# Performance work log

Measured on AMD Instinct MI355X. Metric: run time of the kernel, lower is better.

Reference implementation:

```python
import jax, jax.numpy as jnp
import numpy as np

B, N, D_IN, H, MSG, L, TGT, N_LAYERS = 8, 1024, 64, 128, 128, 5, 12, 3


def setup_inputs() -> dict:
    key = jax.random.key(0)
    ks = jax.random.split(key, 10)
    g = jax.random.uniform(ks[0], (B, N, N), jnp.float32)          # adjacency / edge weights
    h_in = jax.random.uniform(ks[1], (B, N, D_IN), jnp.float32)    # node features (positive -> all nodes present)
    e = jax.random.randint(ks[2], (B, N, N), 0, L).astype(jnp.int32)  # discrete edge labels in [0, L)

    def init(k, shape, fan):
        return jax.random.normal(k, shape, jnp.float32) / np.sqrt(fan)

    A = init(ks[3], (L, H, MSG), H)            # per-edge-label message matrices
    Wi = init(ks[4], (MSG, 3 * H), MSG)        # GRU input weights (r,z,n)
    Wh = init(ks[5], (H, 3 * H), H)            # GRU hidden weights (r,z,n)
    bi = jnp.zeros((3 * H,), jnp.float32)
    bh = jnp.zeros((3 * H,), jnp.float32)
    W_gate = init(ks[6], (2 * H, TGT), 2 * H)  # readout gating net i([h_T, h_0])
    b_gate = jnp.zeros((TGT,), jnp.float32)
    W_out = init(ks[7], (H, TGT), H)           # readout net j(h_T)
    b_out = jnp.zeros((TGT,), jnp.float32)
    return dict(g=g, h_in=h_in, e=e, A=A, Wi=Wi, Wh=Wh, bi=bi, bh=bh,
                W_gate=W_gate, b_gate=b_gate, W_out=W_out, b_out=b_out)


def _gru_step(m, h, Wi, Wh, bi, bh):
    # Single GRU step applied independently per node: m [B,N,MSG], h [B,N,H]
    gi = m @ Wi + bi
    gh = h @ Wh + bh
    i_r, i_z, i_n = jnp.split(gi, 3, axis=-1)
    h_r, h_z, h_n = jnp.split(gh, 3, axis=-1)
    r = jax.nn.sigmoid(i_r + h_r)
    z = jax.nn.sigmoid(i_z + h_z)
    n = jnp.tanh(i_n + r * h_n)
    return (1.0 - z) * n + z * h


def reference(g, h_in, e, A, Wi, Wh, bi, bh, W_gate, b_gate, W_out, b_out):
    n_labels, hidden = A.shape[0], A.shape[1]
    # pad input features with zeros up to hidden_state_size
    h0 = jnp.pad(h_in, ((0, 0), (0, 0), (0, hidden - h_in.shape[-1])))
    # node-presence mask: sum(|h_in|) > 0  -> [B,N,1]
    node_mask = (jnp.sum(jnp.abs(h_in), axis=-1, keepdims=True) > 0).astype(h0.dtype)
    h = h0
    for _ in range(N_LAYERS):  # weight-tied message passing
        # per-label candidate messages: M_l[b,w,:] = h[b,w,:] @ A_l  -> [L,B,N,MSG]
        Ml = jnp.einsum('bwd,ldo->lbwo', h, A)
        agg = jnp.zeros(h.shape[:2] + (A.shape[2],), h.dtype)
        for l in range(n_labels):
            # mask by adjacency AND matching edge label, sum over neighbors w
            w_l = g * (e == l).astype(g.dtype)                  # [B,N,N]
            agg = agg + jnp.einsum('bvw,bwo->bvo', w_l, Ml[l])  # [B,N,MSG]
        h = _gru_step(agg, h, Wi, Wh, bi, bh) * node_mask
    hT = h
    # GGNN readout: sum_v sigmoid(i([h_T, h_0])) * j(h_T), masked on present nodes
    gate = jax.nn.sigmoid(jnp.concatenate([hT, h0], axis=-1) @ W_gate + b_gate)
    out = gate * (hT @ W_out + b_out)                            # [B,N,TGT]
    read_mask = (jnp.sum(h0, axis=-1, keepdims=True) > 0).astype(h0.dtype)
    return jnp.sum(out * read_mask, axis=1)                      # [B,TGT]
```

## Files before the change

### kernel.cpp

```cpp
#include <hip/hip_runtime.h>

#define B_      8
#define N_      1024
#define DIN_    64
#define H_      128
#define MSG2    128
#define L_      5
#define TGT_    12
#define NLAYERS_ 3
#define CAT_    640
#define NODES   (B_ * N_)
#define KSPLIT  4

typedef __attribute__((ext_vector_type(8))) short s16x8;
typedef __attribute__((ext_vector_type(4))) float f32x4;

__device__ __forceinline__ float sigmoidf_(float x) { return 1.f / (1.f + __expf(-x)); }

__device__ __forceinline__ unsigned short f2bf(float x) {
  unsigned int u = __float_as_uint(x);
  u += 0x7FFFu + ((u >> 16) & 1u);
  return (unsigned short)(u >> 16);
}
__device__ __forceinline__ float bf2f(unsigned short u) {
  return __uint_as_float(((unsigned int)u) << 16);
}

__global__ __launch_bounds__(256) void k_prep(const float* __restrict__ h_in,
                                              const float* __restrict__ A,
                                              const float* __restrict__ Wi,
                                              const float* __restrict__ Wh,
                                              float* __restrict__ h,
                                              float* __restrict__ h0,
                                              unsigned short* __restrict__ X,
                                              float* __restrict__ maskA,
                                              float* __restrict__ maskR,
                                              unsigned short* __restrict__ ATh,
                                              unsigned short* __restrict__ ATl,
                                              unsigned short* __restrict__ WiTh,
                                              unsigned short* __restrict__ WiTl,
                                              unsigned short* __restrict__ WhTh,
                                              unsigned short* __restrict__ WhTl) {
  const int blk = blockIdx.x;
  if (blk < NODES / 4) {
    int node = blk * 4 + (threadIdx.x >> 6);
    int lane = threadIdx.x & 63;
    float v = h_in[(size_t)node * DIN_ + lane];
    size_t base = (size_t)node * H_;
    h[base + lane] = v;   h[base + 64 + lane] = 0.f;
    h0[base + lane] = v;  h0[base + 64 + lane] = 0.f;
    unsigned short hi = f2bf(v);
    unsigned short lo = f2bf(v - bf2f(hi));
    size_t xb = (size_t)node * 256;
    X[xb + lane] = hi;        X[xb + 64 + lane] = 0;
    X[xb + 128 + lane] = lo;  X[xb + 192 + lane] = 0;
    float sa = fabsf(v), ss = v;
    for (int off = 32; off > 0; off >>= 1) {
      sa += __shfl_down(sa, off);
      ss += __shfl_down(ss, off);
    }
    if (lane == 0) {
      maskA[node] = (sa > 0.f) ? 1.f : 0.f;
      maskR[node] = (ss > 0.f) ? 1.f : 0.f;
    }
  } else if (blk < NODES / 4 + (CAT_ * 128) / 256) {
    int idx = (blk - NODES / 4) * 256 + threadIdx.x;
    int c = idx >> 7, d = idx & 127;
    int l = c >> 7, o = c & 127;
    float v = A[((size_t)l * 128 + d) * 128 + o];
    unsigned short hi = f2bf(v);
    ATh[idx] = hi;
    ATl[idx] = f2bf(v - bf2f(hi));
  } else {
    int idx = (blk - NODES / 4 - (CAT_ * 128) / 256) * 256 + threadIdx.x;
    if (idx < 384 * 128) {
      int c = idx >> 7, k = idx & 127;
      float v = Wi[(size_t)k * 384 + c];
      unsigned short hi = f2bf(v);
      WiTh[idx] = hi; WiTl[idx] = f2bf(v - bf2f(hi));
    } else {
      int i = idx - 384 * 128;
      int c = i >> 7, k = i & 127;
      float v = Wh[(size_t)k * 384 + c];
      unsigned short hi = f2bf(v);
      WhTh[i] = hi; WhTl[i] = f2bf(v - bf2f(hi));
    }
  }
}

__global__ __launch_bounds__(256) void k_pack(const float* __restrict__ g,
                                              const int* __restrict__ e,
                                              unsigned short* __restrict__ Gb,
                                              unsigned char* __restrict__ Eb) {
  size_t i8 = ((size_t)blockIdx.x * 256 + threadIdx.x) * 8;
  float4 g0 = *(const float4*)&g[i8];
  float4 g1 = *(const float4*)&g[i8 + 4];
  int4   e0 = *(const int4*)&e[i8];
  int4   e1 = *(const int4*)&e[i8 + 4];
  ushort4 ga, gb;
  ga.x = f2bf(g0.x); ga.y = f2bf(g0.y); ga.z = f2bf(g0.z); ga.w = f2bf(g0.w);
  gb.x = f2bf(g1.x); gb.y = f2bf(g1.y); gb.z = f2bf(g1.z); gb.w = f2bf(g1.w);
  *(ushort4*)&Gb[i8]     = ga;
  *(ushort4*)&Gb[i8 + 4] = gb;
  uint2 ev;
  ev.x = (unsigned)(e0.x & 0xFF) | ((unsigned)(e0.y & 0xFF) << 8) |
         ((unsigned)(e0.z & 0xFF) << 16) | ((unsigned)(e0.w & 0xFF) << 24);
  ev.y = (unsigned)(e1.x & 0xFF) | ((unsigned)(e1.y & 0xFF) << 8) |
         ((unsigned)(e1.z & 0xFF) << 16) | ((unsigned)(e1.w & 0xFF) << 24);
  *(uint2*)&Eb[i8] = ev;
}

__global__ __launch_bounds__(256) void k_gemmT(const unsigned short* __restrict__ X,
                                               const unsigned short* __restrict__ ATh,
                                               const unsigned short* __restrict__ ATl,
                                               unsigned short* __restrict__ McatT) {
  __shared__ __align__(16) unsigned short Ah[64 * 40];
  __shared__ __align__(16) unsigned short Al[64 * 40];
  __shared__ __align__(16) unsigned short Bh[128 * 40];
  __shared__ __align__(16) unsigned short Bl2[128 * 40];
  const int tid = threadIdx.x;
  const int c0 = blockIdx.x * 128;
  const int node0 = blockIdx.y * 64;
  const int b = node0 >> 10;
  const int w0 = node0 & 1023;
  const int wid = tid >> 6, lane = tid & 63;
  const int wr = wid >> 1, wc = wid & 1;
  const int lr = lane & 15, lg = lane >> 4;
  const int ar = tid >> 2, aq = (tid & 3) * 8;
  const int br = tid >> 1, bq = (tid & 1) * 16;
  f32x4 acc[2][4];
  #pragma unroll
  for (int m = 0; m < 2; ++m)
    #pragma unroll
    for (int n = 0; n < 4; ++n) acc[m][n] = {0.f, 0.f, 0.f, 0.f};
  for (int kk = 0; kk < 4; ++kk) {
    const int kb = kk * 32;
    *(uint4*)&Ah[ar * 40 + aq] = *(const uint4*)&X[(size_t)(node0 + ar) * 256 + kb + aq];
    *(uint4*)&Al[ar * 40 + aq] = *(const uint4*)&X[(size_t)(node0 + ar) * 256 + 128 + kb + aq];
    const unsigned short* bh = ATh + (size_t)(c0 + br) * 128 + kb + bq;
    const unsigned short* bl = ATl + (size_t)(c0 + br) * 128 + kb + bq;
    *(uint4*)&Bh[br * 40 + bq]      = *(const uint4*)bh;
    *(uint4*)&Bh[br * 40 + bq + 8]  = *(const uint4*)(bh + 8);
    *(uint4*)&Bl2[br * 40 + bq]     = *(const uint4*)bl;
    *(uint4*)&Bl2[br * 40 + bq + 8] = *(const uint4*)(bl + 8);
    __syncthreads();
    s16x8 ah[2], al[2], bhf[4], blf[4];
    #pragma unroll
    for (int m = 0; m < 2; ++m) {
      int row = (wr * 32 + m * 16 + lr) * 40 + lg * 8;
      ah[m] = *(const s16x8*)&Ah[row];
      al[m] = *(const s16x8*)&Al[row];
    }
    #pragma unroll
    for (int n = 0; n < 4; ++n) {
      int row = (wc * 64 + n * 16 + lr) * 40 + lg * 8;
      bhf[n] = *(const s16x8*)&Bh[row];
      blf[n] = *(const s16x8*)&Bl2[row];
    }
    #pragma unroll
    for (int m = 0; m < 2; ++m)
      #pragma unroll
      for (int n = 0; n < 4; ++n) {
        acc[m][n] = __builtin_amdgcn_mfma_f32_16x16x32_bf16(ah[m], bhf[n], acc[m][n], 0, 0, 0);
        acc[m][n] = __builtin_amdgcn_mfma_f32_16x16x32_bf16(ah[m], blf[n], acc[m][n], 0, 0, 0);
        acc[m][n] = __builtin_amdgcn_mfma_f32_16x16x32_bf16(al[m], bhf[n], acc[m][n], 0, 0, 0);
      }
    __syncthreads();
  }
  #pragma unroll
  for (int m = 0; m < 2; ++m)
    #pragma unroll
    for (int n = 0; n < 4; ++n) {
      int c = c0 + wc * 64 + n * 16 + lr;
      int l = c >> 7, o = c & 127;
      int w = w0 + wr * 32 + m * 16 + lg * 4;
      ushort4 v;
      v.x = f2bf(acc[m][n][0]); v.y = f2bf(acc[m][n][1]);
      v.z = f2bf(acc[m][n][2]); v.w = f2bf(acc[m][n][3]);
      *(ushort4*)&McatT[(((size_t)b * L_ + l) * MSG2 + o) * N_ + w] = v;
    }
}

__global__ __launch_bounds__(256, 4) void k_agg_mfma(const unsigned short* __restrict__ Gb,
                                                     const unsigned char* __restrict__ Eb,
                                                     const unsigned short* __restrict__ McatT,
                                                     float* __restrict__ aggP) {
  __shared__ __align__(16) unsigned short Gm[L_][64 * 32];
  __shared__ __align__(16) unsigned short Bl[L_][64 * 32];
  char* GmB = (char*)Gm;
  char* BlB = (char*)Bl;

  const int tid = threadIdx.x;
  const int fid = blockIdx.x;
  const int xcd = fid & 7;
  const int s   = fid >> 3;
  const int p   = xcd * 4 + (s >> 5);
  const int idx = s & 31;
  const int v0  = (idx & 15) * 64;
  const int oh  = idx >> 4;
  const int ks  = p >> 3;
  const int b   = p & 7;

  const int wid  = tid >> 6, lane = tid & 63;
  const int wr   = wid >> 1, wc = wid & 1;
  const int lr   = lane & 15, lg = lane >> 4;

  f32x4 acc[2][2];
  #pragma unroll
  for (int m = 0; m < 2; ++m)
    #pragma unroll
    for (int n = 0; n < 2; ++n) acc[m][n] = {0.f, 0.f, 0.f, 0.f};

  const int ar = tid >> 2, aq = (tid & 3) * 8;
  const int br = tid >> 2, bq = (tid & 3) * 8;
  const size_t garow = ((size_t)b * N_ + v0 + ar) * N_;
  const size_t mrowb = (((size_t)b * L_) * MSG2 + oh * 64 + br) * N_;
  const size_t lstep = (size_t)MSG2 * N_;
  const int ksbase = ks * 256;

  const int gt_w = (ar * 64 + aq * 2) ^ ((ar & 7) << 4);
  const int bl_w = (br * 64 + bq * 2) ^ ((br & 7) << 4);
  const int fsw  = (lr & 7) << 4;

  for (int kk = 0; kk < 8; ++kk) {
    const int kb = ksbase + kk * 32;
    s16x8 gs = *(const s16x8*)&Gb[garow + kb + aq];
    uint2 ev = *(const uint2*)&Eb[garow + kb + aq];
    uint4 bv[L_];
    #pragma unroll
    for (int l = 0; l < L_; ++l)
      bv[l] = *(const uint4*)(McatT + mrowb + (size_t)l * lstep + kb + bq);
    {
      unsigned int w0e = ev.x, w1e = ev.y;
      #pragma unroll
      for (int l = 0; l < L_; ++l) {
        s16x8 mg;
        mg[0] = (((w0e      ) & 0xFFu) == (unsigned)l) ? gs[0] : (short)0;
        mg[1] = (((w0e >>  8) & 0xFFu) == (unsigned)l) ? gs[1] : (short)0;
        mg[2] = (((w0e >> 16) & 0xFFu) == (unsigned)l) ? gs[2] : (short)0;
        mg[3] = (((w0e >> 24) & 0xFFu) == (unsigned)l) ? gs[3] : (short)0;
        mg[4] = (((w1e      ) & 0xFFu) == (unsigned)l) ? gs[4] : (short)0;
        mg[5] = (((w1e >>  8) & 0xFFu) == (unsigned)l) ? gs[5] : (short)0;
        mg[6] = (((w1e >> 16) & 0xFFu) == (unsigned)l) ? gs[6] : (short)0;
        mg[7] = (((w1e >> 24) & 0xFFu) == (unsigned)l) ? gs[7] : (short)0;
        *(s16x8*)(GmB + l * 4096 + gt_w) = mg;
      }
    }
    #pragma unroll
    for (int l = 0; l < L_; ++l)
      *(uint4*)(BlB + l * (64 * 64) + bl_w) = bv[l];
    __syncthreads();

    #pragma unroll
    for (int l = 0; l < L_; ++l) {
      s16x8 af[2], bfr[2];
      #pragma unroll
      for (int m = 0; m < 2; ++m) {
        int row = wr * 32 + m * 16 + lr;
        af[m] = *(const s16x8*)(GmB + l * 4096 + ((row * 64 + lg * 16) ^ fsw));
      }
      #pragma unroll
      for (int n = 0; n < 2; ++n) {
        int row = wc * 32 + n * 16 + lr;
        bfr[n] = *(const s16x8*)(BlB + l * (64 * 64) + ((row * 64 + lg * 16) ^ fsw));
      }
      #pragma unroll
      for (int m = 0; m < 2; ++m)
        #pragma unroll
        for (int n = 0; n < 2; ++n)
          acc[m][n] = __builtin_amdgcn_mfma_f32_16x16x32_bf16(af[m], bfr[n], acc[m][n], 0, 0, 0);
    }
    __syncthreads();
  }

  float* op = aggP + ((size_t)ks * NODES + (size_t)b * N_ + v0) * MSG2 + oh * 64;
  #pragma unroll
  for (int m = 0; m < 2; ++m)
    #pragma unroll
    for (int n = 0; n < 2; ++n)
      #pragma unroll
      for (int j = 0; j < 4; ++j) {
        int row = wr * 32 + m * 16 + lg * 4 + j;
        int col = wc * 32 + n * 16 + lr;
        op[(size_t)row * MSG2 + col] = acc[m][n][j];
      }
}

__global__ __launch_bounds__(256) void k_gates_mfma(const float* __restrict__ aggP,
                                                    const unsigned short* __restrict__ Xh,
                                                    const unsigned short* __restrict__ WiTh,
                                                    const unsigned short* __restrict__ WiTl,
                                                    const unsigned short* __restrict__ WhTh,
                                                    const unsigned short* __restrict__ WhTl,
                                                    float* __restrict__ gates) {
  __shared__ __align__(16) unsigned short Ah[64 * 40];
  __shared__ __align__(16) unsigned short Al[64 * 40];
  __shared__ __align__(16) unsigned short Bh[128 * 40];
  __shared__ __align__(16) unsigned short Bl2[128 * 40];
  const int tid = threadIdx.x;
  const int z = blockIdx.z;
  const unsigned short* WTh = z ? WhTh : WiTh;
  const unsigned short* WTl = z ? WhTl : WiTl;
  const int c0 = blockIdx.x * 128;
  const int node0 = blockIdx.y * 64;
  const int wid = tid >> 6, lane = tid & 63;
  const int wr = wid >> 1, wc = wid & 1;
  const int lr = lane & 15, lg = lane >> 4;
  const int ar = tid >> 2, aq = (tid & 3) * 8;
  const int br = tid >> 1, bq = (tid & 1) * 16;
  const size_t slab = (size_t)NODES * MSG2;
  f32x4 acc[2][4];
  #pragma unroll
  for (int m = 0; m < 2; ++m)
    #pragma unroll
    for (int n = 0; n < 4; ++n) acc[m][n] = {0.f, 0.f, 0.f, 0.f};
  for (int kk = 0; kk < 4; ++kk) {
    const int kb = kk * 32;
    if (z == 0) {
      const float* ap = aggP + (size_t)(node0 + ar) * MSG2 + kb + aq;
      float sv[8] = {0.f, 0.f, 0.f, 0.f, 0.f, 0.f, 0.f, 0.f};
      #pragma unroll
      for (int ss = 0; ss < KSPLIT; ++ss) {
        float4 x0 = *(const float4*)(ap + (size_t)ss * slab);
        float4 x1 = *(const float4*)(ap + (size_t)ss * slab + 4);
        sv[0] += x0.x; sv[1] += x0.y; sv[2] += x0.z; sv[3] += x0.w;
        sv[4] += x1.x; sv[5] += x1.y; sv[6] += x1.z; sv[7] += x1.w;
      }
      s16x8 hv, lv;
      #pragma unroll
      for (int j = 0; j < 8; ++j) {
        unsigned short hi = f2bf(sv[j]);
        hv[j] = (short)hi;
        lv[j] = (short)f2bf(sv[j] - bf2f(hi));
      }
      *(s16x8*)&Ah[ar * 40 + aq] = hv;
      *(s16x8*)&Al[ar * 40 + aq] = lv;
    } else {
      *(uint4*)&Ah[ar * 40 + aq] = *(const uint4*)&Xh[(size_t)(node0 + ar) * 256 + kb + aq];
      *(uint4*)&Al[ar * 40 + aq] = *(const uint4*)&Xh[(size_t)(node0 + ar) * 256 + 128 + kb + aq];
    }
    const unsigned short* bh = WTh + (size_t)(c0 + br) * 128 + kb + bq;
    const unsigned short* bl = WTl + (size_t)(c0 + br) * 128 + kb + bq;
    *(uint4*)&Bh[br * 40 + bq]      = *(const uint4*)bh;
    *(uint4*)&Bh[br * 40 + bq + 8]  = *(const uint4*)(bh + 8);
    *(uint4*)&Bl2[br * 40 + bq]     = *(const uint4*)bl;
    *(uint4*)&Bl2[br * 40 + bq + 8] = *(const uint4*)(bl + 8);
    __syncthreads();
    s16x8 ah[2], al[2], bhf[4], blf[4];
    #pragma unroll
    for (int m = 0; m < 2; ++m) {
      int row = (wr * 32 + m * 16 + lr) * 40 + lg * 8;
      ah[m] = *(const s16x8*)&Ah[row];
      al[m] = *(const s16x8*)&Al[row];
    }
    #pragma unroll
    for (int n = 0; n < 4; ++n) {
      int row = (wc * 64 + n * 16 + lr) * 40 + lg * 8;
      bhf[n] = *(const s16x8*)&Bh[row];
      blf[n] = *(const s16x8*)&Bl2[row];
    }
    #pragma unroll
    for (int m = 0; m < 2; ++m)
      #pragma unroll
      for (int n = 0; n < 4; ++n) {
        acc[m][n] = __builtin_amdgcn_mfma_f32_16x16x32_bf16(ah[m], bhf[n], acc[m][n], 0, 0, 0);
        acc[m][n] = __builtin_amdgcn_mfma_f32_16x16x32_bf16(ah[m], blf[n], acc[m][n], 0, 0, 0);
        acc[m][n] = __builtin_amdgcn_mfma_f32_16x16x32_bf16(al[m], bhf[n], acc[m][n], 0, 0, 0);
      }
    __syncthreads();
  }
  #pragma unroll
  for (int m = 0; m < 2; ++m)
    #pragma unroll
    for (int n = 0; n < 4; ++n) {
      int c = c0 + wc * 64 + n * 16 + lr;
      int row = node0 + wr * 32 + m * 16 + lg * 4;
      #pragma unroll
      for (int j = 0; j < 4; ++j)
        gates[(size_t)(row + j) * 768 + z * 384 + c] = acc[m][n][j];
    }
}

__global__ __launch_bounds__(256) void k_gru_elt(const float* __restrict__ gates,
                                                 const float* __restrict__ bi,
                                                 const float* __restrict__ bh,
                                                 const float* __restrict__ maskA,
                                                 float* __restrict__ h,
                                                 unsigned short* __restrict__ X,
                                                 int writeX) {
  const int t = threadIdx.x;
  const int node = blockIdx.x * 8 + (t >> 5);
  const int j4 = (t & 31) * 4;
  const size_t gb = (size_t)node * 768;
  float4 gir = *(const float4*)&gates[gb + j4];
  float4 giz = *(const float4*)&gates[gb + 128 + j4];
  float4 gin = *(const float4*)&gates[gb + 256 + j4];
  float4 ghr = *(const float4*)&gates[gb + 384 + j4];
  float4 ghz = *(const float4*)&gates[gb + 512 + j4];
  float4 ghn = *(const float4*)&gates[gb + 640 + j4];
  float4 bir = *(const float4*)&bi[j4];
  float4 biz = *(const float4*)&bi[128 + j4];
  float4 bin = *(const float4*)&bi[256 + j4];
  float4 bhr = *(const float4*)&bh[j4];
  float4 bhz = *(const float4*)&bh[128 + j4];
  float4 bhn = *(const float4*)&bh[256 + j4];
  float4 hv = *(const float4*)&h[(size_t)node * 128 + j4];
  float m = maskA[node];
  float4 ho;
  {
    float r = sigmoidf_(gir.x + bir.x + ghr.x + bhr.x);
    float z = sigmoidf_(giz.x + biz.x + ghz.x + bhz.x);
    float nn = tanhf(gin.x + bin.x + r * (ghn.x + bhn.x));
    ho.x = ((1.f - z) * nn + z * hv.x) * m;
  }
  {
    float r = sigmoidf_(gir.y + bir.y + ghr.y + bhr.y);
    float z = sigmoidf_(giz.y + biz.y + ghz.y + bhz.y);
    float nn = tanhf(gin.y + bin.y + r * (ghn.y + bhn.y));
    ho.y = ((1.f - z) * nn + z * hv.y) * m;
  }
  {
    float r = sigmoidf_(gir.z + bir.z + ghr.z + bhr.z);
    float z = sigmoidf_(giz.z + biz.z + ghz.z + bhz.z);
    float nn = tanhf(gin.z + bin.z + r * (ghn.z + bhn.z));
    ho.z = ((1.f - z) * nn + z * hv.z) * m;
  }
  {
    float r = sigmoidf_(gir.w + bir.w + ghr.w + bhr.w);
    float z = sigmoidf_(giz.w + biz.w + ghz.w + bhz.w);
    float nn = tanhf(gin.w + bin.w + r * (ghn.w + bhn.w));
    ho.w = ((1.f - z) * nn + z * hv.w) * m;
  }
  *(float4*)&h[(size_t)node * 128 + j4] = ho;
  if (writeX) {
    ushort4 hi, lo;
    hi.x = f2bf(ho.x); lo.x = f2bf(ho.x - bf2f(hi.x));
    hi.y = f2bf(ho.y); lo.y = f2bf(ho.y - bf2f(hi.y));
    hi.z = f2bf(ho.z); lo.z = f2bf(ho.z - bf2f(hi.z));
    hi.w = f2bf(ho.w); lo.w = f2bf(ho.w - bf2f(hi.w));
    *(ushort4*)&X[(size_t)node * 256 + j4]       = hi;
    *(ushort4*)&X[(size_t)node * 256 + 128 + j4] = lo;
  }
}

__global__ __launch_bounds__(256) void k_readP(const float* __restrict__ h,
                                               const float* __restrict__ h0,
                                               const float* __restrict__ Wg,
                                               const float* __restrict__ Wo,
                                               float* __restrict__ PT) {
  __shared__ float Xt[64][65];
  __shared__ float Wt[64][25];
  const int tid = threadIdx.x;
  const int node0 = blockIdx.x * 64;
  const int row = tid >> 2;
  const int cg  = tid & 3;
  float acc[6] = {0.f, 0.f, 0.f, 0.f, 0.f, 0.f};
  const int sr = tid >> 2;
  const int sk = (tid & 3) * 16;
  #pragma unroll
  for (int kb = 0; kb < 4; ++kb) {
    const float* src = (kb < 2 ? h : h0) + (size_t)(node0 + sr) * 128 + (kb & 1) * 64 + sk;
    #pragma unroll
    for (int q = 0; q < 4; ++q)
      *(float4*)&Xt[sr][sk + q * 4] = *(const float4*)(src + q * 4);
    #pragma unroll
    for (int j = 0; j < 6; ++j) {
      int idx = tid * 6 + j;
      int rk = idx / 24;
      int c24 = idx - rk * 24;
      int gk = kb * 64 + rk;
      float wv;
      if (c24 < 12) wv = Wg[(size_t)gk * TGT_ + c24];
      else          wv = (gk < 128) ? Wo[(size_t)gk * TGT_ + (c24 - 12)] : 0.f;
      Wt[rk][c24] = wv;
    }
    __syncthreads();
    #pragma unroll 8
    for (int k = 0; k < 64; ++k) {
      float x = Xt[row][k];
      #pragma unroll
      for (int j = 0; j < 6; ++j)
        acc[j] += x * Wt[k][cg * 6 + j];
    }
    __syncthreads();
  }
  #pragma unroll
  for (int j = 0; j < 6; ++j)
    PT[(size_t)(cg * 6 + j) * NODES + node0 + row] = acc[j];
}

__global__ __launch_bounds__(256) void k_readR(const float* __restrict__ PT,
                                               const float* __restrict__ maskR,
                                               const float* __restrict__ bg,
                                               const float* __restrict__ bo,
                                               float* __restrict__ out) {
  __shared__ float red[256];
  const int tid = threadIdx.x;
  const int b = blockIdx.x / TGT_;
  const int t = blockIdx.x - b * TGT_;
  const float bgt = bg[t], bot = bo[t];
  float s = 0.f;
  #pragma unroll
  for (int i = 0; i < 4; ++i) {
    int node = b * N_ + i * 256 + tid;
    float p1 = PT[(size_t)t * NODES + node] + bgt;
    float p2 = PT[(size_t)(12 + t) * NODES + node] + bot;
    s += sigmoidf_(p1) * p2 * maskR[node];
  }
  red[tid] = s;
  __syncthreads();
  #pragma unroll
  for (int off = 128; off > 0; off >>= 1) {
    if (tid < off) red[tid] += red[tid + off];
    __syncthreads();
  }
  if (tid == 0) out[b * TGT_ + t] = red[0];
}

extern "C" void kernel_launch(void* const* d_in, const int* in_sizes, int n_in,
                              void* d_out, int out_size, void* d_ws, size_t ws_size,
                              hipStream_t stream) {
  (void)in_sizes; (void)n_in; (void)out_size; (void)ws_size;
  const float* g    = (const float*)d_in[0];
  const float* h_in = (const float*)d_in[1];
  const int*   e    = (const int*)d_in[2];
  const float* A    = (const float*)d_in[3];
  const float* Wi   = (const float*)d_in[4];
  const float* Wh   = (const float*)d_in[5];
  const float* bi   = (const float*)d_in[6];
  const float* bh   = (const float*)d_in[7];
  const float* Wg   = (const float*)d_in[8];
  const float* bg   = (const float*)d_in[9];
  const float* Wo   = (const float*)d_in[10];
  const float* bo   = (const float*)d_in[11];
  float* out = (float*)d_out;
  float* ws  = (float*)d_ws;

  float* h     = ws;
  float* h0    = h + (size_t)NODES * H_;
  float* maskA = h0 + (size_t)NODES * H_;
  float* maskR = maskA + NODES;
  float* PT    = maskR + NODES;
  unsigned short* X    = (unsigned short*)(PT + 24 * NODES);
  unsigned short* ATh  = X + (size_t)NODES * 256;
  unsigned short* ATl  = ATh + CAT_ * 128;
  unsigned short* WiTh = ATl + CAT_ * 128;
  unsigned short* WiTl = WiTh + 384 * 128;
  unsigned short* WhTh = WiTl + 384 * 128;
  unsigned short* WhTl = WhTh + 384 * 128;
  unsigned short* Gb   = WhTl + 384 * 128;
  unsigned char*  Eb   = (unsigned char*)(Gb + (size_t)NODES * N_);
  float* aggP = (float*)(Eb + (size_t)NODES * N_);
  unsigned short* McatT = (unsigned short*)(aggP + (size_t)KSPLIT * NODES * MSG2);
  float* gates = (float*)(McatT + (size_t)B_ * L_ * MSG2 * N_);

  k_prep<<<NODES / 4 + (CAT_ * 128) / 256 + (2 * 384 * 128) / 256, 256, 0, stream>>>(
      h_in, A, Wi, Wh, h, h0, X, maskA, maskR, ATh, ATl, WiTh, WiTl, WhTh, WhTl);
  k_pack<<<(NODES * N_ / 8) / 256, 256, 0, stream>>>(g, e, Gb, Eb);
  for (int layer = 0; layer < NLAYERS_; ++layer) {
    k_gemmT<<<dim3(CAT_ / 128, NODES / 64), 256, 0, stream>>>(X, ATh, ATl, McatT);
    k_agg_mfma<<<(N_ / 64) * 2 * KSPLIT * B_, 256, 0, stream>>>(Gb, Eb, McatT, aggP);
    k_gates_mfma<<<dim3(384 / 128, NODES / 64, 2), 256, 0, stream>>>(aggP, X, WiTh, WiTl, WhTh, WhTl, gates);
    k_gru_elt<<<NODES / 8, 256, 0, stream>>>(gates, bi, bh, maskA, h, X,
                                             (layer < NLAYERS_ - 1) ? 1 : 0);
  }
  k_readP<<<NODES / 64, 256, 0, stream>>>(h, h0, Wg, Wo, PT);
  k_readR<<<B_ * TGT_, 256, 0, stream>>>(PT, maskR, bg, bo, out);
}
```

Measured before the change: 219.7 us.

## Load aggregation MFMA operands directly from global memory, dropping LDS staging

The label-masked aggregation kernel no longer stages masked adjacency and message tiles through shared memory with barriers. Each wave now loads its own MFMA fragments straight from global memory, builds the per-label masked A fragment in registers, and issues the MFMAs with no __syncthreads. This removes LDS traffic and synchronisation. In exchange, operand reuse across waves is lost: each G/E and McatT row is fetched by two waves, which roughly doubles global and L2 loads, and the 4-block occupancy hint is dropped.

```diff
diff --git a/kernel.cpp b/kernel.cpp
--- a/kernel.cpp
+++ b/kernel.cpp
@@ -181,15 +181,10 @@
     }
 }
 
-__global__ __launch_bounds__(256, 4) void k_agg_mfma(const unsigned short* __restrict__ Gb,
-                                                     const unsigned char* __restrict__ Eb,
-                                                     const unsigned short* __restrict__ McatT,
-                                                     float* __restrict__ aggP) {
-  __shared__ __align__(16) unsigned short Gm[L_][64 * 32];
-  __shared__ __align__(16) unsigned short Bl[L_][64 * 32];
-  char* GmB = (char*)Gm;
-  char* BlB = (char*)Bl;
-
+__global__ __launch_bounds__(256) void k_agg_reg(const unsigned short* __restrict__ Gb,
+                                                 const unsigned char* __restrict__ Eb,
+                                                 const unsigned short* __restrict__ McatT,
+                                                 float* __restrict__ aggP) {
   const int tid = threadIdx.x;
   const int fid = blockIdx.x;
   const int xcd = fid & 7;
@@ -201,9 +196,10 @@
   const int ks  = p >> 3;
   const int b   = p & 7;
 
-  const int wid  = tid >> 6, lane = tid & 63;
-  const int wr   = wid >> 1, wc = wid & 1;
-  const int lr   = lane & 15, lg = lane >> 4;
+  const int wid = tid >> 6, lane = tid & 63;
+  const int vw = v0 + (wid & 1) * 32;
+  const int ow = oh * 64 + (wid >> 1) * 32;
+  const int lr = lane & 15, lg = lane >> 4;
 
   f32x4 acc[2][2];
   #pragma unroll
@@ -211,77 +207,63 @@
     #pragma unroll
     for (int n = 0; n < 2; ++n) acc[m][n] = {0.f, 0.f, 0.f, 0.f};
 
-  const int ar = tid >> 2, aq = (tid & 3) * 8;
-  const int br = tid >> 2, bq = (tid & 3) * 8;
-  const size_t garow = ((size_t)b * N_ + v0 + ar) * N_;
-  const size_t mrowb = (((size_t)b * L_) * MSG2 + oh * 64 + br) * N_;
-  const size_t lstep = (size_t)MSG2 * N_;
-  const int ksbase = ks * 256;
-
-  const int gt_w = (ar * 64 + aq * 2) ^ ((ar & 7) << 4);
-  const int bl_w = (br * 64 + bq * 2) ^ ((br & 7) << 4);
-  const int fsw  = (lr & 7) << 4;
+  const int kb0 = ks * 256 + lg * 8;
+  size_t gOff0 = ((size_t)b * N_ + vw + lr) * N_ + kb0;
+  size_t gOff1 = gOff0 + (size_t)16 * N_;
+  size_t bOff  = (((size_t)b * L_) * MSG2 + ow + lr) * N_ + kb0;
+  const size_t nStep = (size_t)16 * N_;
+  const size_t lStep = (size_t)MSG2 * N_;
 
   for (int kk = 0; kk < 8; ++kk) {
-    const int kb = ksbase + kk * 32;
-    s16x8 gs = *(const s16x8*)&Gb[garow + kb + aq];
-    uint2 ev = *(const uint2*)&Eb[garow + kb + aq];
-    uint4 bv[L_];
-    #pragma unroll
-    for (int l = 0; l < L_; ++l)
-      bv[l] = *(const uint4*)(McatT + mrowb + (size_t)l * lstep + kb + bq);
-    {
-      unsigned int w0e = ev.x, w1e = ev.y;
-      #pragma unroll
-      for (int l = 0; l < L_; ++l) {
-        s16x8 mg;
-        mg[0] = (((w0e      ) & 0xFFu) == (unsigned)l) ? gs[0] : (short)0;
-        mg[1] = (((w0e >>  8) & 0xFFu) == (unsigned)l) ? gs[1] : (short)0;
-        mg[2] = (((w0e >> 16) & 0xFFu) == (unsigned)l) ? gs[2] : (short)0;
-        mg[3] = (((w0e >> 24) & 0xFFu) == (unsigned)l) ? gs[3] : (short)0;
-        mg[4] = (((w1e      ) & 0xFFu) == (unsigned)l) ? gs[4] : (short)0;
-        mg[5] = (((w1e >>  8) & 0xFFu) == (unsigned)l) ? gs[5] : (short)0;
-        mg[6] = (((w1e >> 16) & 0xFFu) == (unsigned)l) ? gs[6] : (short)0;
-        mg[7] = (((w1e >> 24) & 0xFFu) == (unsigned)l) ? gs[7] : (short)0;
-        *(s16x8*)(GmB + l * 4096 + gt_w) = mg;
-      }
-    }
-    #pragma unroll
-    for (int l = 0; l < L_; ++l)
-      *(uint4*)(BlB + l * (64 * 64) + bl_w) = bv[l];
-    __syncthreads();
-
+    s16x8 gs0 = *(const s16x8*)(Gb + gOff0);
+    s16x8 gs1 = *(const s16x8*)(Gb + gOff1);
+    uint2 es0 = *(const uint2*)(Eb + gOff0);
+    uint2 es1 = *(const uint2*)(Eb + gOff1);
     #pragma unroll
     for (int l = 0; l < L_; ++l) {
-      s16x8 af[2], bfr[2];
-      #pragma unroll
-      for (int m = 0; m < 2; ++m) {
-        int row = wr * 32 + m * 16 + lr;
-        af[m] = *(const s16x8*)(GmB + l * 4096 + ((row * 64 + lg * 16) ^ fsw));
-      }
-      #pragma unroll
-      for (int n = 0; n < 2; ++n) {
-        int row = wc * 32 + n * 16 + lr;
-        bfr[n] = *(const s16x8*)(BlB + l * (64 * 64) + ((row * 64 + lg * 16) ^ fsw));
-      }
-      #pragma unroll
-      for (int m = 0; m < 2; ++m)
-        #pragma unroll
-        for (int n = 0; n < 2; ++n)
-          acc[m][n] = __builtin_amdgcn_mfma_f32_16x16x32_bf16(af[m], bfr[n], acc[m][n], 0, 0, 0);
-    }
-    __syncthreads();
-  }
-
-  float* op = aggP + ((size_t)ks * NODES + (size_t)b * N_ + v0) * MSG2 + oh * 64;
+      s16x8 bf0 = *(const s16x8*)(McatT + bOff + (size_t)l * lStep);
+      s16x8 bf1 = *(const s16x8*)(McatT + bOff + (size_t)l * lStep + nStep);
+      {
+        unsigned int w0e = es0.x, w1e = es0.y;
+        s16x8 af;
+        af[0] = (((w0e      ) & 0xFFu) == (unsigned)l) ? gs0[0] : (short)0;
+        af[1] = (((w0e >>  8) & 0xFFu) == (unsigned)l) ? gs0[1] : (short)0;
+        af[2] = (((w0e >> 16) & 0xFFu) == (unsigned)l) ? gs0[2] : (short)0;
+        af[3] = (((w0e >> 24) & 0xFFu) == (unsigned)l) ? gs0[3] : (short)0;
+        af[4] = (((w1e      ) & 0xFFu) == (unsigned)l) ? gs0[4] : (short)0;
+        af[5] = (((w1e >>  8) & 0xFFu) == (unsigned)l) ? gs0[5] : (short)0;
+        af[6] = (((w1e >> 16) & 0xFFu) == (unsigned)l) ? gs0[6] : (short)0;
+        af[7] = (((w1e >> 24) & 0xFFu) == (unsigned)l) ? gs0[7] : (short)0;
+        acc[0][0] = __builtin_amdgcn_mfma_f32_16x16x32_bf16(af, bf0, acc[0][0], 0, 0, 0);
+        acc[0][1] = __builtin_amdgcn_mfma_f32_16x16x32_bf16(af, bf1, acc[0][1], 0, 0, 0);
+      }
+      {
+        unsigned int w0e = es1.x, w1e = es1.y;
+        s16x8 af;
+        af[0] = (((w0e      ) & 0xFFu) == (unsigned)l) ? gs1[0] : (short)0;
+        af[1] = (((w0e >>  8) & 0xFFu) == (unsigned)l) ? gs1[1] : (short)0;
+        af[2] = (((w0e >> 16) & 0xFFu) == (unsigned)l) ? gs1[2] : (short)0;
+        af[3] = (((w0e >> 24) & 0xFFu) == (unsigned)l) ? gs1[3] : (short)0;
+        af[4] = (((w1e      ) & 0xFFu) == (unsigned)l) ? gs1[4] : (short)0;
+        af[5] = (((w1e >>  8) & 0xFFu) == (unsigned)l) ? gs1[5] : (short)0;
+        af[6] = (((w1e >> 16) & 0xFFu) == (unsigned)l) ? gs1[6] : (short)0;
+        af[7] = (((w1e >> 24) & 0xFFu) == (unsigned)l) ? gs1[7] : (short)0;
+        acc[1][0] = __builtin_amdgcn_mfma_f32_16x16x32_bf16(af, bf0, acc[1][0], 0, 0, 0);
+        acc[1][1] = __builtin_amdgcn_mfma_f32_16x16x32_bf16(af, bf1, acc[1][1], 0, 0, 0);
+      }
+    }
+    gOff0 += 32; gOff1 += 32; bOff += 32;
+  }
+
+  float* op = aggP + ((size_t)ks * NODES + (size_t)b * N_) * MSG2;
   #pragma unroll
   for (int m = 0; m < 2; ++m)
     #pragma unroll
     for (int n = 0; n < 2; ++n)
       #pragma unroll
       for (int j = 0; j < 4; ++j) {
-        int row = wr * 32 + m * 16 + lg * 4 + j;
-        int col = wc * 32 + n * 16 + lr;
+        int row = vw + m * 16 + lg * 4 + j;
+        int col = ow + n * 16 + lr;
         op[(size_t)row * MSG2 + col] = acc[m][n][j];
       }
 }
@@ -559,7 +541,7 @@
   k_pack<<<(NODES * N_ / 8) / 256, 256, 0, stream>>>(g, e, Gb, Eb);
   for (int layer = 0; layer < NLAYERS_; ++layer) {
     k_gemmT<<<dim3(CAT_ / 128, NODES / 64), 256, 0, stream>>>(X, ATh, ATl, McatT);
-    k_agg_mfma<<<(N_ / 64) * 2 * KSPLIT * B_, 256, 0, stream>>>(Gb, Eb, McatT, aggP);
+    k_agg_reg<<<(N_ / 64) * 2 * KSPLIT * B_, 256, 0, stream>>>(Gb, Eb, McatT, aggP);
     k_gates_mfma<<<dim3(384 / 128, NODES / 64, 2), 256, 0, stream>>>(aggP, X, WiTh, WiTl, WhTh, WhTl, gates);
     k_gru_elt<<<NODES / 8, 256, 0, stream>>>(gates, bi, bh, maskA, h, X,
                                              (layer < NLAYERS_ - 1) ? 1 : 0);
```

Measured after the change: 306.5 us. +39.5%, slower.
